# Performance work log

Measured on AMD Instinct MI355X. Metric: run time of the kernel, lower is better.

Reference implementation:

```python
import jax, jax.numpy as jnp
import numpy as np
import math

D_MODEL = 512
DIM_K = 512
DIM_V = 512
N_HEADS = 8
B, S = 2, 2048


def setup_inputs() -> dict:
    key = jax.random.key(0)
    ks = jax.random.split(key, 10)
    s = 1.0 / math.sqrt(D_MODEL)
    return {
        "x": jax.random.normal(ks[0], (B, S, D_MODEL), jnp.float32),
        "y": jax.random.normal(ks[1], (B, S, D_MODEL), jnp.float32),
        # torch nn.Linear weights: [out, in]
        "q_w": jax.random.normal(ks[2], (DIM_K, D_MODEL), jnp.float32) * s,
        "q_b": jax.random.normal(ks[3], (DIM_K,), jnp.float32) * s,
        "k_w": jax.random.normal(ks[4], (DIM_K, D_MODEL), jnp.float32) * s,
        "k_b": jax.random.normal(ks[5], (DIM_K,), jnp.float32) * s,
        "v_w": jax.random.normal(ks[6], (DIM_V, D_MODEL), jnp.float32) * s,
        "v_b": jax.random.normal(ks[7], (DIM_V,), jnp.float32) * s,
        "o_w": jax.random.normal(ks[8], (D_MODEL, DIM_V), jnp.float32) * s,
        "o_b": jax.random.normal(ks[9], (D_MODEL,), jnp.float32) * s,
    }


def reference(x, y, q_w, q_b, k_w, k_b, v_w, v_b, o_w, o_b):
    b, s, _ = x.shape
    hd_k = DIM_K // N_HEADS
    hd_v = DIM_V // N_HEADS
    norm_fact = 1.0 / math.sqrt(D_MODEL)  # note: original scales by 1/sqrt(d_model)
    # torch code reshapes the flat [B,S,dim] projection row-major into [H,B,S,hd]
    Q = (x @ q_w.T + q_b).reshape(N_HEADS, b, s, hd_k)
    K = (y @ k_w.T + k_b).reshape(N_HEADS, b, s, hd_k)
    V = (y @ v_w.T + v_b).reshape(N_HEADS, b, s, hd_v)
    # scores: [H, B, Sq, Sk]
    scores = jnp.einsum("hbqd,hbkd->hbqk", Q, K) * norm_fact
    # per-row mean threshold: mask (set -inf) where score <= row mean
    thre = jnp.mean(scores, axis=-1, keepdims=True)
    scores = jnp.where(scores <= thre, -jnp.inf, scores)
    attn = jax.nn.softmax(scores, axis=-1)
    out = jnp.einsum("hbqk,hbkd->hbqd", attn, V).reshape(b, s, DIM_V)
    return out @ o_w.T + o_b
```

## Files before the change

### kernel.cpp

```cpp
#include <hip/hip_runtime.h>


typedef unsigned short ushort;
typedef unsigned int uint;

typedef __bf16  bf16x8   __attribute__((ext_vector_type(8)));
typedef float   floatx4  __attribute__((ext_vector_type(4)));
typedef float   floatx16 __attribute__((ext_vector_type(16)));
typedef float   float4v  __attribute__((ext_vector_type(4)));
typedef uint    uint4v   __attribute__((ext_vector_type(4)));
typedef ushort  ushort4v __attribute__((ext_vector_type(4)));

#define MFMA16(a,b,c) __builtin_amdgcn_mfma_f32_16x16x32_bf16((a),(b),(c),0,0,0)
#define MFMA32(a,b,c) __builtin_amdgcn_mfma_f32_32x32x16_bf16((a),(b),(c),0,0,0)

__device__ __forceinline__ float b2f(ushort u){
  union { uint i; float f; } v; v.i = ((uint)u) << 16; return v.f;
}
__device__ __forceinline__ ushort f2b(float f){
  union { float f; uint i; } v; v.f = f;
  uint r = v.i + 0x7FFFu + ((v.i >> 16) & 1u);
  return (ushort)(r >> 16);
}
__device__ __forceinline__ void split2(float f, ushort& h, ushort& l){
  h = f2b(f);
  l = f2b(f - b2f(h));
}
__device__ __forceinline__ void gload16(const ushort* g, ushort* l){
  __builtin_amdgcn_global_load_lds(
      (const __attribute__((address_space(1))) unsigned int*)g,
      (__attribute__((address_space(3))) unsigned int*)l, 16, 0, 0);
}

__global__ __launch_bounds__(256) void split_xy(
    const float* __restrict__ x, const float* __restrict__ y,
    ushort* __restrict__ xhi, ushort* __restrict__ xlo,
    ushort* __restrict__ yhi, ushort* __restrict__ ylo)
{
  int idx = blockIdx.x * 256 + threadIdx.x;
  const float* sp; ushort *hp, *lp; int i;
  if (idx < 524288){ sp = x; hp = xhi; lp = xlo; i = idx; }
  else             { sp = y; hp = yhi; lp = ylo; i = idx - 524288; }
  float4v d = ((const float4v*)sp)[i];
  ushort4v h, l;
  #pragma unroll
  for (int j=0;j<4;j++){ ushort hh,ll; split2(d[j],hh,ll); h[j]=hh; l[j]=ll; }
  ((ushort4v*)hp)[i] = h;
  ((ushort4v*)lp)[i] = l;
}

__global__ __launch_bounds__(256) void split_w(
    const float* __restrict__ qw, const float* __restrict__ kw,
    const float* __restrict__ vw, const float* __restrict__ ow,
    ushort* __restrict__ qwh, ushort* __restrict__ qwl,
    ushort* __restrict__ kwh, ushort* __restrict__ kwl,
    ushort* __restrict__ vwh, ushort* __restrict__ owh)
{
  int idx = blockIdx.x * 256 + threadIdx.x;
  int a = idx >> 16, i = idx & 65535;
  if (a < 2){
    const float* sp = a ? kw : qw;
    ushort *hp = a ? kwh : qwh, *lp = a ? kwl : qwl;
    float4v d = ((const float4v*)sp)[i];
    ushort4v h, l;
    #pragma unroll
    for (int j=0;j<4;j++){ ushort hh,ll; split2(d[j],hh,ll); h[j]=hh; l[j]=ll; }
    ((ushort4v*)hp)[i] = h;
    ((ushort4v*)lp)[i] = l;
  } else {
    const float* sp = (a == 2) ? vw : ow;
    ushort *hp = (a == 2) ? vwh : owh;
    float4v d = ((const float4v*)sp)[i];
    ushort4v h;
    #pragma unroll
    for (int j=0;j<4;j++) h[j] = f2b(d[j]);
    ((ushort4v*)hp)[i] = h;
  }
}

template<int OUT_MODE, bool KSUM, int PREC>
__global__ __launch_bounds__(256) void proj2(
    const ushort* __restrict__ Ahi, const ushort* __restrict__ Alo,
    const ushort* __restrict__ Bhi, const ushort* __restrict__ Blo,
    const float* __restrict__ bias,
    float* __restrict__ outf, ushort* __restrict__ outhi, ushort* __restrict__ outlo,
    float* __restrict__ ksum_out)
{
  constexpr bool SA = (PREC == 2);
  const int id = blockIdx.x;
  const int m0 = ((id & 7) * 8 + ((id >> 3) & 7)) * 64;
  const int n0 = (id >> 6) * 64;

  __shared__ __align__(16) ushort AH[2][4096];
  __shared__ __align__(16) ushort AL[SA?2:1][4096];
  __shared__ __align__(16) ushort BH[2][4096];
  __shared__ __align__(16) ushort BL[SA?2:1][4096];
  __shared__ float cs[64];

  const int t    = threadIdx.x;
  const int lane = t & 63;
  const int w    = t >> 6;
  const int wm   = w >> 1, wn = w & 1;
  const int lr   = lane & 15, lg = lane >> 4;

  const int rl  = lane >> 3;
  const int c8s = (lane & 7) ^ rl;
  constexpr int NCH = SA ? 8 : 4;

  auto stage = [&](int buf, int k0){
    #pragma unroll
    for (int j = 0; j < NCH; j++){
      const int c = w * NCH + j;
      if constexpr (SA){
        if (c < 8)
          gload16(Ahi + (size_t)(m0 + c*8 + rl)*512 + k0 + c8s*8, &AH[buf][c*512]);
        else if (c < 16)
          gload16(Alo + (size_t)(m0 + (c-8)*8 + rl)*512 + k0 + c8s*8, &AL[buf][(c-8)*512]);
        else if (c < 24)
          gload16(Bhi + (size_t)(n0 + (c-16)*8 + rl)*512 + k0 + c8s*8, &BH[buf][(c-16)*512]);
        else
          gload16(Blo + (size_t)(n0 + (c-24)*8 + rl)*512 + k0 + c8s*8, &BL[buf][(c-24)*512]);
      } else {
        if (c < 8)
          gload16(Ahi + (size_t)(m0 + c*8 + rl)*512 + k0 + c8s*8, &AH[buf][c*512]);
        else
          gload16(Bhi + (size_t)(n0 + (c-8)*8 + rl)*512 + k0 + c8s*8, &BH[buf][(c-8)*512]);
      }
    }
  };

  floatx4 zf; zf[0]=0.f; zf[1]=0.f; zf[2]=0.f; zf[3]=0.f;
  floatx4 acc[2][2];
  #pragma unroll
  for (int i=0;i<2;i++)
    #pragma unroll
    for (int j=0;j<2;j++) acc[i][j] = zf;

  stage(0, 0);
  __syncthreads();

  int cur = 0;
  for (int it = 0; it < 8; ++it){
    if (it < 7) stage(cur^1, (it+1)*64);

    const ushort* AHc = AH[cur];
    const ushort* ALc = SA ? AL[cur] : nullptr;
    const ushort* BHc = BH[cur];
    const ushort* BLc = SA ? BL[cur] : nullptr;

    #pragma unroll
    for (int ks=0; ks<2; ks++){
      const int xo = ((ks*4 + lg) ^ (lr & 7)) << 3;
      bf16x8 ah[2], al[2], bh[2], bl[2];
      #pragma unroll
      for (int mi=0;mi<2;mi++){
        const int off = (wm*32 + mi*16 + lr)*64 + xo;
        ah[mi] = *(const bf16x8*)&AHc[off];
        if constexpr (SA) al[mi] = *(const bf16x8*)&ALc[off];
      }
      #pragma unroll
      for (int ni=0;ni<2;ni++){
        const int off = (wn*32 + ni*16 + lr)*64 + xo;
        bh[ni] = *(const bf16x8*)&BHc[off];
        if constexpr (SA) bl[ni] = *(const bf16x8*)&BLc[off];
      }
      #pragma unroll
      for (int mi=0;mi<2;mi++)
        #pragma unroll
        for (int ni=0;ni<2;ni++){
          acc[mi][ni] = MFMA16(ah[mi], bh[ni], acc[mi][ni]);
          if constexpr (SA){
            acc[mi][ni] = MFMA16(ah[mi], bl[ni], acc[mi][ni]);
            acc[mi][ni] = MFMA16(al[mi], bh[ni], acc[mi][ni]);
          }
        }
    }
    __syncthreads();
    cur ^= 1;
  }

  #pragma unroll
  for (int ni=0;ni<2;ni++){
    const int n = n0 + wn*32 + ni*16 + lr;
    const float bn = bias[n];
    #pragma unroll
    for (int mi=0;mi<2;mi++){
      #pragma unroll
      for (int r=0;r<4;r++){
        const int m = m0 + wm*32 + mi*16 + lg*4 + r;
        const float c = acc[mi][ni][r] + bn;
        const size_t off = (size_t)m*512 + n;
        if (OUT_MODE == 0)      { outf[off] = c; }
        else if (OUT_MODE == 1) { ushort h,l; split2(c,h,l); outhi[off]=h; outlo[off]=l; }
        else                    { outhi[off] = f2b(c); }
      }
    }
  }

  if (KSUM) {
    if (t < 64) cs[t] = 0.f;
    __syncthreads();
    #pragma unroll
    for (int ni=0;ni<2;ni++){
      float s = 0.f;
      #pragma unroll
      for (int mi=0;mi<2;mi++)
        #pragma unroll
        for (int r=0;r<4;r++) s += acc[mi][ni][r];
      atomicAdd(&cs[wn*32 + ni*16 + lr], s);
    }
    __syncthreads();
    if (t < 64){
      const int hb = m0 >> 8;
      atomicAdd(&ksum_out[hb*64 + t], cs[t] + 64.f * bias[n0 + t]);
    }
  }
}

__global__ __launch_bounds__(256) void vtrans(
    const ushort* __restrict__ pv, ushort* __restrict__ vt)
{
  const int hb = blockIdx.y;
  const int s0 = blockIdx.x * 64;
  const size_t cb = (size_t)hb * 131072;
  __shared__ __align__(16) ushort T[64][68];
  const int t = threadIdx.x;
  {
    int s = t >> 2, c = (t & 3) * 16;
    *(uint4v*)&T[s][c]     = *(const uint4v*)&pv[cb + (size_t)(s0+s)*64 + c];
    *(uint4v*)&T[s][c + 8] = *(const uint4v*)&pv[cb + (size_t)(s0+s)*64 + c + 8];
  }
  __syncthreads();
  const int d = t >> 2, sc = (t & 3) * 16;
  ushort buf[16];
  #pragma unroll
  for (int i=0;i<16;i++) buf[i] = T[sc + i][d];
  *(uint4v*)&vt[cb + (size_t)d*2048 + s0 + sc]     = *(const uint4v*)&buf[0];
  *(uint4v*)&vt[cb + (size_t)d*2048 + s0 + sc + 8] = *(const uint4v*)&buf[8];
}

__device__ __forceinline__ void stage_khvt(
    ushort* khb, ushort* vtb, const ushort* gkhi, const ushort* gvt,
    size_t cb, int kvb, int ws, int l)
{
  const int rsub = l >> 3;
  const int c8   = (l & 7) ^ rsub;
  #pragma unroll
  for (int j = 0; j < 4; j++){
    const int chunk = ws*4 + j;
    const int a   = chunk >> 3;
    const int sub = chunk & 7;
    const int row = sub*8 + rsub;
    if (a == 0)
      gload16(gkhi + cb + (size_t)(kvb + row)*64 + c8*8, khb + sub*512);
    else
      gload16(gvt  + cb + (size_t)row*2048 + kvb + c8*8, vtb + sub*512);
  }
}
__device__ __forceinline__ void stage_kl(
    ushort* klb, const ushort* gklo, size_t cb, int kvb, int ws, int l)
{
  const int rsub = l >> 3;
  const int c8   = (l & 7) ^ rsub;
  #pragma unroll
  for (int j = 0; j < 2; j++){
    const int sub = ws*2 + j;
    const int row = sub*8 + rsub;
    gload16(gklo + cb + (size_t)(kvb + row)*64 + c8*8, klb + sub*512);
  }
}

__global__ __launch_bounds__(512) void attn_kernel(
    const ushort* __restrict__ qhi, const ushort* __restrict__ qlo,
    const ushort* __restrict__ khi, const ushort* __restrict__ klo,
    const ushort* __restrict__ vt,  const float* __restrict__ ksum,
    ushort* __restrict__ Oa, ushort* __restrict__ Ob,
    float* __restrict__ za, float* __restrict__ zb)
{
  const int id = blockIdx.x;
  const int hb = ((id & 7) << 1) | ((id >> 3) & 1);
  const int kv = (id >> 4) & 1;
  const int q0 = (id >> 5) * 128;
  const size_t cb = (size_t)hb * 131072;
  const float C1 = 0.04419417382415922f * 1.44269504088896f;

  __shared__ __align__(16) ushort SMEM[40960];
  ushort* KHb = SMEM;
  ushort* VTb = SMEM + 16384;
  ushort* KLb = SMEM + 32768;

  const int t = threadIdx.x, l = t & 63, w = t >> 6;
  const int half = w >> 2, ws = w & 3;
  const int lq = l & 31, h = l >> 5;
  const int kbase = kv*1024 + half*512;

  ushort* op = kv ? Ob : Oa;
  float*  zp = kv ? zb : za;

  stage_khvt(KHb + (half*2)*4096, VTb + (half*2)*4096, khi, vt, cb, kbase, ws, l);
  stage_kl(KLb + half*4096, klo, cb, kbase, ws, l);

  union U8 { bf16x8 v; ushort u[8]; };
  U8 qfh[4], qfl[4];
  float part = 0.f;
  #pragma unroll
  for (int st=0; st<4; st++){
    size_t g = cb + (size_t)(q0 + ws*32 + lq)*64 + st*16 + h*8;
    qfh[st].v = *(const bf16x8*)&qhi[g];
    qfl[st].v = *(const bf16x8*)&qlo[g];
    float4v k0 = *(const float4v*)&ksum[hb*64 + st*16 + h*8];
    float4v k1 = *(const float4v*)&ksum[hb*64 + st*16 + h*8 + 4];
    #pragma unroll
    for (int j=0;j<4;j++) part += (b2f(qfh[st].u[j])   + b2f(qfl[st].u[j]))   * k0[j];
    #pragma unroll
    for (int j=0;j<4;j++) part += (b2f(qfh[st].u[4+j]) + b2f(qfl[st].u[4+j])) * k1[j];
  }
  part += __shfl_xor(part, 32);
  const float rm = part * (1.f/2048.f);
  const float nrmc = -rm * C1;

  floatx16 O0 = {0,0,0,0,0,0,0,0,0,0,0,0,0,0,0,0};
  floatx16 O1 = O0;
  float za_r = 0.f, zb_r = 0.f;

  __syncthreads();

  for (int kt = 0; kt < 8; kt++){
    const int cur = kt & 1;
    if (kt + 1 < 8)
      stage_khvt(KHb + (half*2 + (cur^1))*4096, VTb + (half*2 + (cur^1))*4096,
                 khi, vt, cb, kbase + (kt+1)*64, ws, l);

    const ushort* KHc = KHb + (half*2 + cur)*4096;
    const ushort* KLc = KLb + half*4096;
    const ushort* VTc = VTb + (half*2 + cur)*4096;

    floatx16 s0 = {0,0,0,0,0,0,0,0,0,0,0,0,0,0,0,0};
    floatx16 s1 = s0;
    #pragma unroll
    for (int st=0; st<4; st++){
      const int xo = (((st*2 + h) ^ (lq & 7)) << 3);
      bf16x8 kh0 = *(const bf16x8*)&KHc[(lq     )*64 + xo];
      bf16x8 kl0 = *(const bf16x8*)&KLc[(lq     )*64 + xo];
      bf16x8 kh1 = *(const bf16x8*)&KHc[(32 + lq)*64 + xo];
      bf16x8 kl1 = *(const bf16x8*)&KLc[(32 + lq)*64 + xo];
      s0 = MFMA32(kh0, qfh[st].v, s0);
      s1 = MFMA32(kh1, qfh[st].v, s1);
      s0 = MFMA32(kh0, qfl[st].v, s0);
      s1 = MFMA32(kh1, qfl[st].v, s1);
      s0 = MFMA32(kl0, qfh[st].v, s0);
      s1 = MFMA32(kl1, qfh[st].v, s1);
    }
    __syncthreads();
    if (kt + 1 < 8)
      stage_kl(KLb + half*4096, klo, cb, kbase + (kt+1)*64, ws, l);

    #pragma unroll
    for (int r=0;r<16;r++){
      float t0 = __builtin_fmaf(s0[r], C1, nrmc);
      float t1 = __builtin_fmaf(s1[r], C1, nrmc);
      float e0 = __builtin_amdgcn_exp2f(t0);
      float e1 = __builtin_amdgcn_exp2f(t1);
      e0 = (t0 > 0.f) ? e0 : 0.f;
      e1 = (t1 > 0.f) ? e1 : 0.f;
      za_r += e0; zb_r += e1;
      s0[r] = e0; s1[r] = e1;
    }

    bf16x8 pa[4];
    #pragma unroll
    for (int g=0; g<2; g++){
      const floatx16& sp = g ? s1 : s0;
      #pragma unroll
      for (int sg=0; sg<2; sg++){
        uint X0,X1,X2,X3;
        asm("v_cvt_pk_bf16_f32 %0, %1, %2" : "=v"(X0) : "v"(sp[sg*8+0]), "v"(sp[sg*8+1]));
        asm("v_cvt_pk_bf16_f32 %0, %1, %2" : "=v"(X1) : "v"(sp[sg*8+2]), "v"(sp[sg*8+3]));
        asm("v_cvt_pk_bf16_f32 %0, %1, %2" : "=v"(X2) : "v"(sp[sg*8+4]), "v"(sp[sg*8+5]));
        asm("v_cvt_pk_bf16_f32 %0, %1, %2" : "=v"(X3) : "v"(sp[sg*8+6]), "v"(sp[sg*8+7]));
        asm("v_permlane32_swap_b32 %0, %1" : "+v"(X0), "+v"(X2));
        asm("v_permlane32_swap_b32 %0, %1" : "+v"(X1), "+v"(X3));
        union { uint u[4]; bf16x8 v; } pu;
        pu.u[0]=X0; pu.u[1]=X1; pu.u[2]=X2; pu.u[3]=X3;
        pa[g*2+sg] = pu.v;
      }
    }

    #pragma unroll
    for (int s4=0; s4<4; s4++){
      const int xo = (((s4*2 + h) ^ (lq & 7)) << 3);
      bf16x8 vf0 = *(const bf16x8*)&VTc[(lq     )*64 + xo];
      bf16x8 vf1 = *(const bf16x8*)&VTc[(32 + lq)*64 + xo];
      O0 = MFMA32(pa[s4], vf0, O0);
      O1 = MFMA32(pa[s4], vf1, O1);
    }

    __syncthreads();
  }

  float zacc = za_r + zb_r;
  zacc += __shfl_xor(zacc, 32);
  float* CB = (float*)SMEM;
  const int ci = (ws*64 + l)*34;
  if (half == 1){
    #pragma unroll
    for (int i=0;i<16;i++){ CB[ci+i] = O0[i]; CB[ci+16+i] = O1[i]; }
    CB[ci+32] = zacc;
  }
  __syncthreads();
  if (half == 0){
    const float zsum = zacc + CB[ci+32];
    if (h == 0) zp[hb*2048 + q0 + ws*32 + l] = zsum;
    #pragma unroll
    for (int r=0;r<16;r++){ O0[r] += CB[ci+r]; O1[r] += CB[ci+16+r]; }
    #pragma unroll
    for (int r=0;r<16;r++){
      const int crow = (r&3) + ((r>>2)<<3) + (h<<2);
      const int q = q0 + ws*32 + crow;
      const size_t base = cb + (size_t)q*64 + lq;
      op[base]      = f2b(O0[r]);
      op[base + 32] = f2b(O1[r]);
    }
  }
}

__global__ __launch_bounds__(256) void combine_kernel(
    const ushort* __restrict__ Oa, const ushort* __restrict__ Ob,
    const float* __restrict__ za, const float* __restrict__ zb,
    ushort* __restrict__ attno)
{
  const int idx = blockIdx.x * 256 + threadIdx.x;
  const int q = idx >> 3;
  const float zi = 1.f / (za[q] + zb[q]);
  uint4v av = ((const uint4v*)Oa)[idx];
  uint4v bv = ((const uint4v*)Ob)[idx];
  uint4v ov;
  #pragma unroll
  for (int j=0;j<4;j++){
    float lo = (b2f((ushort)(av[j] & 0xffff)) + b2f((ushort)(bv[j] & 0xffff))) * zi;
    float hi = (b2f((ushort)(av[j] >> 16))    + b2f((ushort)(bv[j] >> 16)))    * zi;
    ov[j] = (uint)f2b(lo) | ((uint)f2b(hi) << 16);
  }
  ((uint4v*)attno)[idx] = ov;
}

extern "C" void kernel_launch(void* const* d_in, const int* in_sizes, int n_in,
                              void* d_out, int out_size, void* d_ws, size_t ws_size,
                              hipStream_t stream)
{
  const float* x   = (const float*)d_in[0];
  const float* y   = (const float*)d_in[1];
  const float* q_w = (const float*)d_in[2];
  const float* q_b = (const float*)d_in[3];
  const float* k_w = (const float*)d_in[4];
  const float* k_b = (const float*)d_in[5];
  const float* v_w = (const float*)d_in[6];
  const float* v_b = (const float*)d_in[7];
  const float* o_w = (const float*)d_in[8];
  const float* o_b = (const float*)d_in[9];

  const size_t NE = 4096ull * 512;
  const size_t WN = 512ull * 512;
  ushort* p = (ushort*)d_ws;
  ushort* pq_hi = p;
  ushort* pq_lo = pq_hi + NE;
  ushort* pk_hi = pq_lo + NE;
  ushort* pk_lo = pk_hi + NE;
  ushort* pv    = pk_lo + NE;
  ushort* xhi   = pv + NE;
  ushort* xlo   = xhi + NE;
  ushort* yhi   = xlo + NE;
  ushort* ylo   = yhi + NE;
  ushort* vtg   = xhi;
  ushort* attno = xlo;
  ushort* Oa    = pv;
  ushort* Ob    = yhi;
  float*  za    = (float*)ylo;
  float*  zb    = za + 32768;
  ushort* qwh = ylo + NE;
  ushort* qwl = qwh + WN;
  ushort* kwh = qwl + WN;
  ushort* kwl = kwh + WN;
  ushort* vwh = kwl + WN;
  ushort* owh = vwh + WN;
  float*  ksumb = (float*)(owh + WN);

  hipMemsetAsync(ksumb, 0, 16 * 64 * sizeof(float), stream);

  split_xy<<<4096, 256, 0, stream>>>(x, y, xhi, xlo, yhi, ylo);
  split_w <<<1024, 256, 0, stream>>>(q_w, k_w, v_w, o_w,
                                     qwh, qwl, kwh, kwl, vwh, owh);

  proj2<1,false,2><<<512, 256, 0, stream>>>(xhi, xlo, qwh, qwl, q_b, nullptr, pq_hi, pq_lo, nullptr);
  proj2<1,true ,2><<<512, 256, 0, stream>>>(yhi, ylo, kwh, kwl, k_b, nullptr, pk_hi, pk_lo, ksumb);
  proj2<2,false,0><<<512, 256, 0, stream>>>(yhi, nullptr, vwh, nullptr, v_b, nullptr, pv, nullptr, nullptr);
  vtrans<<<dim3(32,16), 256, 0, stream>>>(pv, vtg);
  attn_kernel<<<512, 512, 0, stream>>>(pq_hi, pq_lo, pk_hi, pk_lo, vtg, ksumb,
                                       Oa, Ob, za, zb);
  combine_kernel<<<1024, 256, 0, stream>>>(Oa, Ob, za, zb, attno);
  proj2<0,false,0><<<512, 256, 0, stream>>>(attno, nullptr, owh, nullptr, o_b, (float*)d_out, nullptr, nullptr, nullptr);
}
```

Measured before the change: 110.7 us.

## Merge split kernels, batch QKV projections, fuse combine into output projection

Merges the two fp32-to-bf16 split kernels into one launch and the three Q/K/V projection launches into a single 1536-block grid that picks operands per segment at run time. The combine step (sum of the two KV halves and normalisation) now runs inside the output projection's A-tile load, so the attno intermediate is never written or re-read. The attention kernel's LDS plan changes: V^T is single-buffered and loaded per tile, shrinking shared memory from 40960 to 32768 ushorts, which may allow more resident blocks but exposes V load latency. The trade-offs are runtime branching and maximum-size LDS in the merged projection kernel, plus less latency hiding for V.

Measured after the change: 107.3 us. -3.0%, faster.

```diff
diff --git a/kernel.cpp b/kernel.cpp
--- a/kernel.cpp
+++ b/kernel.cpp
@@ -32,35 +32,21 @@
       (__attribute__((address_space(3))) unsigned int*)l, 16, 0, 0);
 }
 
-__global__ __launch_bounds__(256) void split_xy(
+__global__ __launch_bounds__(256) void split_all(
     const float* __restrict__ x, const float* __restrict__ y,
-    ushort* __restrict__ xhi, ushort* __restrict__ xlo,
-    ushort* __restrict__ yhi, ushort* __restrict__ ylo)
-{
-  int idx = blockIdx.x * 256 + threadIdx.x;
-  const float* sp; ushort *hp, *lp; int i;
-  if (idx < 524288){ sp = x; hp = xhi; lp = xlo; i = idx; }
-  else             { sp = y; hp = yhi; lp = ylo; i = idx - 524288; }
-  float4v d = ((const float4v*)sp)[i];
-  ushort4v h, l;
-  #pragma unroll
-  for (int j=0;j<4;j++){ ushort hh,ll; split2(d[j],hh,ll); h[j]=hh; l[j]=ll; }
-  ((ushort4v*)hp)[i] = h;
-  ((ushort4v*)lp)[i] = l;
-}
-
-__global__ __launch_bounds__(256) void split_w(
     const float* __restrict__ qw, const float* __restrict__ kw,
     const float* __restrict__ vw, const float* __restrict__ ow,
+    ushort* __restrict__ xhi, ushort* __restrict__ xlo,
+    ushort* __restrict__ yhi, ushort* __restrict__ ylo,
     ushort* __restrict__ qwh, ushort* __restrict__ qwl,
     ushort* __restrict__ kwh, ushort* __restrict__ kwl,
     ushort* __restrict__ vwh, ushort* __restrict__ owh)
 {
   int idx = blockIdx.x * 256 + threadIdx.x;
-  int a = idx >> 16, i = idx & 65535;
-  if (a < 2){
-    const float* sp = a ? kw : qw;
-    ushort *hp = a ? kwh : qwh, *lp = a ? kwl : qwl;
+  if (idx < 1048576){
+    const float* sp; ushort *hp, *lp; int i;
+    if (idx < 524288){ sp = x; hp = xhi; lp = xlo; i = idx; }
+    else             { sp = y; hp = yhi; lp = ylo; i = idx - 524288; }
     float4v d = ((const float4v*)sp)[i];
     ushort4v h, l;
     #pragma unroll
@@ -68,33 +54,59 @@
     ((ushort4v*)hp)[i] = h;
     ((ushort4v*)lp)[i] = l;
   } else {
-    const float* sp = (a == 2) ? vw : ow;
-    ushort *hp = (a == 2) ? vwh : owh;
-    float4v d = ((const float4v*)sp)[i];
-    ushort4v h;
-    #pragma unroll
-    for (int j=0;j<4;j++) h[j] = f2b(d[j]);
-    ((ushort4v*)hp)[i] = h;
-  }
-}
-
-template<int OUT_MODE, bool KSUM, int PREC>
-__global__ __launch_bounds__(256) void proj2(
-    const ushort* __restrict__ Ahi, const ushort* __restrict__ Alo,
-    const ushort* __restrict__ Bhi, const ushort* __restrict__ Blo,
-    const float* __restrict__ bias,
-    float* __restrict__ outf, ushort* __restrict__ outhi, ushort* __restrict__ outlo,
-    float* __restrict__ ksum_out)
-{
-  constexpr bool SA = (PREC == 2);
-  const int id = blockIdx.x;
+    int k = idx - 1048576;
+    int a = k >> 16, i = k & 65535;
+    if (a < 2){
+      const float* sp = a ? kw : qw;
+      ushort *hp = a ? kwh : qwh, *lp = a ? kwl : qwl;
+      float4v d = ((const float4v*)sp)[i];
+      ushort4v h, l;
+      #pragma unroll
+      for (int j=0;j<4;j++){ ushort hh,ll; split2(d[j],hh,ll); h[j]=hh; l[j]=ll; }
+      ((ushort4v*)hp)[i] = h;
+      ((ushort4v*)lp)[i] = l;
+    } else {
+      const float* sp = (a == 2) ? vw : ow;
+      ushort *hp = (a == 2) ? vwh : owh;
+      float4v d = ((const float4v*)sp)[i];
+      ushort4v h;
+      #pragma unroll
+      for (int j=0;j<4;j++) h[j] = f2b(d[j]);
+      ((ushort4v*)hp)[i] = h;
+    }
+  }
+}
+
+__global__ __launch_bounds__(256) void proj_qkv(
+    const ushort* __restrict__ xhi, const ushort* __restrict__ xlo,
+    const ushort* __restrict__ yhi, const ushort* __restrict__ ylo,
+    const ushort* __restrict__ qwh, const ushort* __restrict__ qwl,
+    const ushort* __restrict__ kwh, const ushort* __restrict__ kwl,
+    const ushort* __restrict__ vwh,
+    const float* __restrict__ q_b, const float* __restrict__ k_b,
+    const float* __restrict__ v_b,
+    ushort* __restrict__ pq_hi, ushort* __restrict__ pq_lo,
+    ushort* __restrict__ pk_hi, ushort* __restrict__ pk_lo,
+    ushort* __restrict__ pv, float* __restrict__ ksum_out)
+{
+  const int seg = blockIdx.x >> 9;
+  const int id  = blockIdx.x & 511;
   const int m0 = ((id & 7) * 8 + ((id >> 3) & 7)) * 64;
   const int n0 = (id >> 6) * 64;
+  const bool split = (seg < 2);
+
+  const ushort* Ahi = (seg == 0) ? xhi : yhi;
+  const ushort* Alo = (seg == 0) ? xlo : ylo;
+  const ushort* Bhi = (seg == 0) ? qwh : ((seg == 1) ? kwh : vwh);
+  const ushort* Blo = (seg == 0) ? qwl : kwl;
+  const float*  bias = (seg == 0) ? q_b : ((seg == 1) ? k_b : v_b);
+  ushort* outhi = (seg == 0) ? pq_hi : ((seg == 1) ? pk_hi : pv);
+  ushort* outlo = (seg == 0) ? pq_lo : pk_lo;
 
   __shared__ __align__(16) ushort AH[2][4096];
-  __shared__ __align__(16) ushort AL[SA?2:1][4096];
+  __shared__ __align__(16) ushort AL[2][4096];
   __shared__ __align__(16) ushort BH[2][4096];
-  __shared__ __align__(16) ushort BL[SA?2:1][4096];
+  __shared__ __align__(16) ushort BL[2][4096];
   __shared__ float cs[64];
 
   const int t    = threadIdx.x;
@@ -105,13 +117,12 @@
 
   const int rl  = lane >> 3;
   const int c8s = (lane & 7) ^ rl;
-  constexpr int NCH = SA ? 8 : 4;
 
   auto stage = [&](int buf, int k0){
-    #pragma unroll
-    for (int j = 0; j < NCH; j++){
-      const int c = w * NCH + j;
-      if constexpr (SA){
+    if (split){
+      #pragma unroll
+      for (int j = 0; j < 8; j++){
+        const int c = w * 8 + j;
         if (c < 8)
           gload16(Ahi + (size_t)(m0 + c*8 + rl)*512 + k0 + c8s*8, &AH[buf][c*512]);
         else if (c < 16)
@@ -120,7 +131,11 @@
           gload16(Bhi + (size_t)(n0 + (c-16)*8 + rl)*512 + k0 + c8s*8, &BH[buf][(c-16)*512]);
         else
           gload16(Blo + (size_t)(n0 + (c-24)*8 + rl)*512 + k0 + c8s*8, &BL[buf][(c-24)*512]);
-      } else {
+      }
+    } else {
+      #pragma unroll
+      for (int j = 0; j < 4; j++){
+        const int c = w * 4 + j;
         if (c < 8)
           gload16(Ahi + (size_t)(m0 + c*8 + rl)*512 + k0 + c8s*8, &AH[buf][c*512]);
         else
@@ -143,11 +158,6 @@
   for (int it = 0; it < 8; ++it){
     if (it < 7) stage(cur^1, (it+1)*64);
 
-    const ushort* AHc = AH[cur];
-    const ushort* ALc = SA ? AL[cur] : nullptr;
-    const ushort* BHc = BH[cur];
-    const ushort* BLc = SA ? BL[cur] : nullptr;
-
     #pragma unroll
     for (int ks=0; ks<2; ks++){
       const int xo = ((ks*4 + lg) ^ (lr & 7)) << 3;
@@ -155,21 +165,21 @@
       #pragma unroll
       for (int mi=0;mi<2;mi++){
         const int off = (wm*32 + mi*16 + lr)*64 + xo;
-        ah[mi] = *(const bf16x8*)&AHc[off];
-        if constexpr (SA) al[mi] = *(const bf16x8*)&ALc[off];
+        ah[mi] = *(const bf16x8*)&AH[cur][off];
+        if (split) al[mi] = *(const bf16x8*)&AL[cur][off];
       }
       #pragma unroll
       for (int ni=0;ni<2;ni++){
         const int off = (wn*32 + ni*16 + lr)*64 + xo;
-        bh[ni] = *(const bf16x8*)&BHc[off];
-        if constexpr (SA) bl[ni] = *(const bf16x8*)&BLc[off];
+        bh[ni] = *(const bf16x8*)&BH[cur][off];
+        if (split) bl[ni] = *(const bf16x8*)&BL[cur][off];
       }
       #pragma unroll
       for (int mi=0;mi<2;mi++)
         #pragma unroll
         for (int ni=0;ni<2;ni++){
           acc[mi][ni] = MFMA16(ah[mi], bh[ni], acc[mi][ni]);
-          if constexpr (SA){
+          if (split){
             acc[mi][ni] = MFMA16(ah[mi], bl[ni], acc[mi][ni]);
             acc[mi][ni] = MFMA16(al[mi], bh[ni], acc[mi][ni]);
           }
@@ -190,14 +200,13 @@
         const int m = m0 + wm*32 + mi*16 + lg*4 + r;
         const float c = acc[mi][ni][r] + bn;
         const size_t off = (size_t)m*512 + n;
-        if (OUT_MODE == 0)      { outf[off] = c; }
-        else if (OUT_MODE == 1) { ushort h,l; split2(c,h,l); outhi[off]=h; outlo[off]=l; }
-        else                    { outhi[off] = f2b(c); }
-      }
-    }
-  }
-
-  if (KSUM) {
+        if (split){ ushort h,l; split2(c,h,l); outhi[off]=h; outlo[off]=l; }
+        else      { outhi[off] = f2b(c); }
+      }
+    }
+  }
+
+  if (seg == 1) {
     if (t < 64) cs[t] = 0.f;
     __syncthreads();
     #pragma unroll
@@ -239,26 +248,8 @@
   *(uint4v*)&vt[cb + (size_t)d*2048 + s0 + sc + 8] = *(const uint4v*)&buf[8];
 }
 
-__device__ __forceinline__ void stage_khvt(
-    ushort* khb, ushort* vtb, const ushort* gkhi, const ushort* gvt,
-    size_t cb, int kvb, int ws, int l)
-{
-  const int rsub = l >> 3;
-  const int c8   = (l & 7) ^ rsub;
-  #pragma unroll
-  for (int j = 0; j < 4; j++){
-    const int chunk = ws*4 + j;
-    const int a   = chunk >> 3;
-    const int sub = chunk & 7;
-    const int row = sub*8 + rsub;
-    if (a == 0)
-      gload16(gkhi + cb + (size_t)(kvb + row)*64 + c8*8, khb + sub*512);
-    else
-      gload16(gvt  + cb + (size_t)row*2048 + kvb + c8*8, vtb + sub*512);
-  }
-}
-__device__ __forceinline__ void stage_kl(
-    ushort* klb, const ushort* gklo, size_t cb, int kvb, int ws, int l)
+__device__ __forceinline__ void stage_kh(
+    ushort* dst, const ushort* gk, size_t cb, int kvb, int ws, int l)
 {
   const int rsub = l >> 3;
   const int c8   = (l & 7) ^ rsub;
@@ -266,7 +257,19 @@
   for (int j = 0; j < 2; j++){
     const int sub = ws*2 + j;
     const int row = sub*8 + rsub;
-    gload16(gklo + cb + (size_t)(kvb + row)*64 + c8*8, klb + sub*512);
+    gload16(gk + cb + (size_t)(kvb + row)*64 + c8*8, dst + sub*512);
+  }
+}
+__device__ __forceinline__ void stage_vt(
+    ushort* dst, const ushort* gvt, size_t cb, int kvb, int ws, int l)
+{
+  const int rsub = l >> 3;
+  const int c8   = (l & 7) ^ rsub;
+  #pragma unroll
+  for (int j = 0; j < 2; j++){
+    const int sub = ws*2 + j;
+    const int row = sub*8 + rsub;
+    gload16(gvt + cb + (size_t)row*2048 + kvb + c8*8, dst + sub*512);
   }
 }
 
@@ -284,10 +287,7 @@
   const size_t cb = (size_t)hb * 131072;
   const float C1 = 0.04419417382415922f * 1.44269504088896f;
 
-  __shared__ __align__(16) ushort SMEM[40960];
-  ushort* KHb = SMEM;
-  ushort* VTb = SMEM + 16384;
-  ushort* KLb = SMEM + 32768;
+  __shared__ __align__(16) ushort SMEM[32768];
 
   const int t = threadIdx.x, l = t & 63, w = t >> 6;
   const int half = w >> 2, ws = w & 3;
@@ -297,8 +297,13 @@
   ushort* op = kv ? Ob : Oa;
   float*  zp = kv ? zb : za;
 
-  stage_khvt(KHb + (half*2)*4096, VTb + (half*2)*4096, khi, vt, cb, kbase, ws, l);
-  stage_kl(KLb + half*4096, klo, cb, kbase, ws, l);
+  ushort* KH0 = SMEM + (half*2)*4096;
+  ushort* KH1 = SMEM + (half*2+1)*4096;
+  ushort* VTB = SMEM + 16384 + half*4096;
+  ushort* KLB = SMEM + 24576 + half*4096;
+
+  stage_kh(KH0, khi, cb, kbase, ws, l);
+  stage_kh(KLB, klo, cb, kbase, ws, l);
 
   union U8 { bf16x8 v; ushort u[8]; };
   U8 qfh[4], qfl[4];
@@ -326,14 +331,10 @@
   __syncthreads();
 
   for (int kt = 0; kt < 8; kt++){
-    const int cur = kt & 1;
-    if (kt + 1 < 8)
-      stage_khvt(KHb + (half*2 + (cur^1))*4096, VTb + (half*2 + (cur^1))*4096,
-                 khi, vt, cb, kbase + (kt+1)*64, ws, l);
-
-    const ushort* KHc = KHb + (half*2 + cur)*4096;
-    const ushort* KLc = KLb + half*4096;
-    const ushort* VTc = VTb + (half*2 + cur)*4096;
+    ushort* KHc = (kt & 1) ? KH1 : KH0;
+    ushort* KHn = (kt & 1) ? KH0 : KH1;
+    if (kt + 1 < 8) stage_kh(KHn, khi, cb, kbase + (kt+1)*64, ws, l);
+    stage_vt(VTB, vt, cb, kbase + kt*64, ws, l);
 
     floatx16 s0 = {0,0,0,0,0,0,0,0,0,0,0,0,0,0,0,0};
     floatx16 s1 = s0;
@@ -341,9 +342,9 @@
     for (int st=0; st<4; st++){
       const int xo = (((st*2 + h) ^ (lq & 7)) << 3);
       bf16x8 kh0 = *(const bf16x8*)&KHc[(lq     )*64 + xo];
-      bf16x8 kl0 = *(const bf16x8*)&KLc[(lq     )*64 + xo];
+      bf16x8 kl0 = *(const bf16x8*)&KLB[(lq     )*64 + xo];
       bf16x8 kh1 = *(const bf16x8*)&KHc[(32 + lq)*64 + xo];
-      bf16x8 kl1 = *(const bf16x8*)&KLc[(32 + lq)*64 + xo];
+      bf16x8 kl1 = *(const bf16x8*)&KLB[(32 + lq)*64 + xo];
       s0 = MFMA32(kh0, qfh[st].v, s0);
       s1 = MFMA32(kh1, qfh[st].v, s1);
       s0 = MFMA32(kh0, qfl[st].v, s0);
@@ -352,8 +353,7 @@
       s1 = MFMA32(kl1, qfh[st].v, s1);
     }
     __syncthreads();
-    if (kt + 1 < 8)
-      stage_kl(KLb + half*4096, klo, cb, kbase + (kt+1)*64, ws, l);
+    if (kt + 1 < 8) stage_kh(KLB, klo, cb, kbase + (kt+1)*64, ws, l);
 
     #pragma unroll
     for (int r=0;r<16;r++){
@@ -389,8 +389,8 @@
     #pragma unroll
     for (int s4=0; s4<4; s4++){
       const int xo = (((s4*2 + h) ^ (lq & 7)) << 3);
-      bf16x8 vf0 = *(const bf16x8*)&VTc[(lq     )*64 + xo];
-      bf16x8 vf1 = *(const bf16x8*)&VTc[(32 + lq)*64 + xo];
+      bf16x8 vf0 = *(const bf16x8*)&VTB[(lq     )*64 + xo];
+      bf16x8 vf1 = *(const bf16x8*)&VTB[(32 + lq)*64 + xo];
       O0 = MFMA32(pa[s4], vf0, O0);
       O1 = MFMA32(pa[s4], vf1, O1);
     }
@@ -424,24 +424,115 @@
   }
 }
 
-__global__ __launch_bounds__(256) void combine_kernel(
+__global__ __launch_bounds__(256) void proj_out(
     const ushort* __restrict__ Oa, const ushort* __restrict__ Ob,
     const float* __restrict__ za, const float* __restrict__ zb,
-    ushort* __restrict__ attno)
-{
-  const int idx = blockIdx.x * 256 + threadIdx.x;
-  const int q = idx >> 3;
-  const float zi = 1.f / (za[q] + zb[q]);
-  uint4v av = ((const uint4v*)Oa)[idx];
-  uint4v bv = ((const uint4v*)Ob)[idx];
-  uint4v ov;
-  #pragma unroll
-  for (int j=0;j<4;j++){
-    float lo = (b2f((ushort)(av[j] & 0xffff)) + b2f((ushort)(bv[j] & 0xffff))) * zi;
-    float hi = (b2f((ushort)(av[j] >> 16))    + b2f((ushort)(bv[j] >> 16)))    * zi;
-    ov[j] = (uint)f2b(lo) | ((uint)f2b(hi) << 16);
-  }
-  ((uint4v*)attno)[idx] = ov;
+    const ushort* __restrict__ owh, const float* __restrict__ o_b,
+    float* __restrict__ outf)
+{
+  const int id = blockIdx.x;
+  const int m0 = ((id & 7) * 8 + ((id >> 3) & 7)) * 64;
+  const int n0 = (id >> 6) * 64;
+
+  __shared__ __align__(16) ushort AH[2][4096];
+  __shared__ __align__(16) ushort BH[2][4096];
+
+  const int t    = threadIdx.x;
+  const int lane = t & 63;
+  const int w    = t >> 6;
+  const int wm   = w >> 1, wn = w & 1;
+  const int lr   = lane & 15, lg = lane >> 4;
+
+  const int rl  = lane >> 3;
+  const int c8s = (lane & 7) ^ rl;
+
+  auto stageB = [&](int buf, int k0){
+    #pragma unroll
+    for (int j = 0; j < 2; j++){
+      const int c = w*2 + j;
+      gload16(owh + (size_t)(n0 + c*8 + rl)*512 + k0 + c8s*8, &BH[buf][c*512]);
+    }
+  };
+
+  const int ar = t >> 2, ac = t & 3;
+  uint4v la0, la1, lb0, lb1;
+  auto issueA = [&](int k0){
+    const size_t base = (size_t)(m0 + ar)*512 + k0 + ac*16;
+    la0 = *(const uint4v*)&Oa[base];
+    la1 = *(const uint4v*)&Oa[base + 8];
+    lb0 = *(const uint4v*)&Ob[base];
+    lb1 = *(const uint4v*)&Ob[base + 8];
+  };
+  auto writeA = [&](int buf, int k0){
+    const int m = m0 + ar;
+    const int zq = (m >> 8)*2048 + (m & 255)*8 + (k0 >> 6);
+    const float zi = 1.f / (za[zq] + zb[zq]);
+    uint4v o0, o1;
+    #pragma unroll
+    for (int j=0;j<4;j++){
+      float l0 = (b2f((ushort)(la0[j] & 0xffff)) + b2f((ushort)(lb0[j] & 0xffff))) * zi;
+      float h0 = (b2f((ushort)(la0[j] >> 16))    + b2f((ushort)(lb0[j] >> 16)))    * zi;
+      o0[j] = (uint)f2b(l0) | ((uint)f2b(h0) << 16);
+      float l1 = (b2f((ushort)(la1[j] & 0xffff)) + b2f((ushort)(lb1[j] & 0xffff))) * zi;
+      float h1 = (b2f((ushort)(la1[j] >> 16))    + b2f((ushort)(lb1[j] >> 16)))    * zi;
+      o1[j] = (uint)f2b(l1) | ((uint)f2b(h1) << 16);
+    }
+    const int p0 = ar*64 + (((ac*2    ) ^ (ar & 7)) << 3);
+    const int p1 = ar*64 + (((ac*2 + 1) ^ (ar & 7)) << 3);
+    *(uint4v*)&AH[buf][p0] = o0;
+    *(uint4v*)&AH[buf][p1] = o1;
+  };
+
+  floatx4 zf; zf[0]=0.f; zf[1]=0.f; zf[2]=0.f; zf[3]=0.f;
+  floatx4 acc[2][2];
+  #pragma unroll
+  for (int i=0;i<2;i++)
+    #pragma unroll
+    for (int j=0;j<2;j++) acc[i][j] = zf;
+
+  issueA(0);
+  stageB(0, 0);
+  writeA(0, 0);
+  __syncthreads();
+
+  int cur = 0;
+  for (int it = 0; it < 8; ++it){
+    if (it < 7){ issueA((it+1)*64); stageB(cur^1, (it+1)*64); }
+
+    #pragma unroll
+    for (int ks=0; ks<2; ks++){
+      const int xo = ((ks*4 + lg) ^ (lr & 7)) << 3;
+      bf16x8 ah[2], bh[2];
+      #pragma unroll
+      for (int mi=0;mi<2;mi++)
+        ah[mi] = *(const bf16x8*)&AH[cur][(wm*32 + mi*16 + lr)*64 + xo];
+      #pragma unroll
+      for (int ni=0;ni<2;ni++)
+        bh[ni] = *(const bf16x8*)&BH[cur][(wn*32 + ni*16 + lr)*64 + xo];
+      #pragma unroll
+      for (int mi=0;mi<2;mi++)
+        #pragma unroll
+        for (int ni=0;ni<2;ni++)
+          acc[mi][ni] = MFMA16(ah[mi], bh[ni], acc[mi][ni]);
+    }
+    if (it < 7) writeA(cur^1, (it+1)*64);
+    __syncthreads();
+    cur ^= 1;
+  }
+
+  #pragma unroll
+  for (int ni=0;ni<2;ni++){
+    const int n = n0 + wn*32 + ni*16 + lr;
+    const float bn = o_b[n];
+    #pragma unroll
+    for (int mi=0;mi<2;mi++){
+      #pragma unroll
+      for (int r=0;r<4;r++){
+        const int m = m0 + wm*32 + mi*16 + lg*4 + r;
+        outf[(size_t)m*512 + n] = acc[mi][ni][r] + bn;
+      }
+    }
+  }
 }
 
 extern "C" void kernel_launch(void* const* d_in, const int* in_sizes, int n_in,
@@ -472,7 +563,6 @@
   ushort* yhi   = xlo + NE;
   ushort* ylo   = yhi + NE;
   ushort* vtg   = xhi;
-  ushort* attno = xlo;
   ushort* Oa    = pv;
   ushort* Ob    = yhi;
   float*  za    = (float*)ylo;
@@ -487,16 +577,15 @@
 
   hipMemsetAsync(ksumb, 0, 16 * 64 * sizeof(float), stream);
 
-  split_xy<<<4096, 256, 0, stream>>>(x, y, xhi, xlo, yhi, ylo);
-  split_w <<<1024, 256, 0, stream>>>(q_w, k_w, v_w, o_w,
-                                     qwh, qwl, kwh, kwl, vwh, owh);
-
-  proj2<1,false,2><<<512, 256, 0, stream>>>(xhi, xlo, qwh, qwl, q_b, nullptr, pq_hi, pq_lo, nullptr);
-  proj2<1,true ,2><<<512, 256, 0, stream>>>(yhi, ylo, kwh, kwl, k_b, nullptr, pk_hi, pk_lo, ksumb);
-  proj2<2,false,0><<<512, 256, 0, stream>>>(yhi, nullptr, vwh, nullptr, v_b, nullptr, pv, nullptr, nullptr);
+  split_all<<<5120, 256, 0, stream>>>(x, y, q_w, k_w, v_w, o_w,
+                                      xhi, xlo, yhi, ylo,
+                                      qwh, qwl, kwh, kwl, vwh, owh);
+  proj_qkv<<<1536, 256, 0, stream>>>(xhi, xlo, yhi, ylo,
+                                     qwh, qwl, kwh, kwl, vwh,
+                                     q_b, k_b, v_b,
+                                     pq_hi, pq_lo, pk_hi, pk_lo, pv, ksumb);
   vtrans<<<dim3(32,16), 256, 0, stream>>>(pv, vtg);
   attn_kernel<<<512, 512, 0, stream>>>(pq_hi, pq_lo, pk_hi, pk_lo, vtg, ksumb,
                                        Oa, Ob, za, zb);
-  combine_kernel<<<1024, 256, 0, stream>>>(Oa, Ob, za, zb, attno);
-  proj2<0,false,0><<<512, 256, 0, stream>>>(attno, nullptr, owh, nullptr, o_b, (float*)d_out, nullptr, nullptr, nullptr);
-}
+  proj_out<<<512, 256, 0, stream>>>(Oa, Ob, za, zb, owh, o_b, (float*)d_out);
+}
```
